# Kernel tuning notes

Hardware: AMD Instinct MI355X
Metric: run time of the kernel (lower is better)

## Reference

```python
import jax, jax.numpy as jnp
import numpy as np

NEG_SLOPE = 0.01  # torch nn.LeakyReLU default

B, N, IN_F, OUT_F, HEADS = 4, 2048, 512, 512, 8
D = OUT_F // HEADS  # 64


def setup_inputs() -> dict:
    key = jax.random.key(0)
    ks = jax.random.split(key, 4)
    X = jax.random.normal(ks[0], (B, N, IN_F), dtype=jnp.float32)
    W_v = jax.random.normal(ks[1], (IN_F, D), dtype=jnp.float32) * (IN_F ** -0.5)
    b_v = jnp.zeros((D,), dtype=jnp.float32)
    W_q = jax.random.normal(ks[2], (D, HEADS), dtype=jnp.float32) * (D ** -0.5)
    b_q = jnp.zeros((HEADS,), dtype=jnp.float32)
    W_k = jax.random.normal(ks[3], (D, HEADS), dtype=jnp.float32) * (D ** -0.5)
    b_k = jnp.zeros((HEADS,), dtype=jnp.float32)
    return {"X": X, "W_v": W_v, "b_v": b_v, "W_q": W_q, "b_q": b_q, "W_k": W_k, "b_k": b_k}


def reference(X, W_v, b_v, W_q, b_q, W_k, b_k):
    # V: (B, N, D)
    V = X @ W_v + b_v
    # per-node, per-head scalar scores: (B, N, H) -> (B, H, N)
    Q = jnp.swapaxes(V @ W_q + b_q, 1, 2)
    K = jnp.swapaxes(V @ W_k + b_k, 1, 2)
    # A[b,h,i,j] = leaky_relu(Q[b,h,j] + K[b,h,i])  (broadcast outer-sum)
    A = jax.nn.leaky_relu(Q[:, :, None, :] + K[:, :, :, None], negative_slope=NEG_SLOPE)
    A = jax.nn.softmax(A, axis=-1)  # dropout = identity in eval mode
    # H[b,i,h,f] = sum_j A[b,h,i,j] V[b,j,f]
    H = jnp.einsum('bhij,bjf->bihf', A, V)
    return H.reshape(H.shape[0], H.shape[1], -1)  # (B, N, H*D)
```

## Files before the change

### kernel.cpp

```cpp
#include <hip/hip_runtime.h>

#define BB   4
#define NN   2048
#define INF  512
#define HH   8
#define DD   64
#define BH   (BB*HH)
#define NCK  16
#define CKS  128
#define KSP  2


__global__ __launch_bounds__(256) void k_v(
    const float* __restrict__ X, const float* __restrict__ Wv,
    float* __restrict__ Vpart)
{
  __shared__ float Ws[64][68];
  const int t  = threadIdx.x;
  const int tc = t & 15;
  const int tr = t >> 4;
  const int rg = blockIdx.x >> 1;
  const int kh = blockIdx.x & 1;
  const int r0 = rg * 32;
  const int k0 = kh * 256;
  float acc[2][4] = {{0.f}};

  for (int kc = 0; kc < 256; kc += 64) {
    __syncthreads();
    #pragma unroll
    for (int i = 0; i < 4; i++) {
      const int e4 = t + i * 256;
      const int k  = e4 >> 4;
      const int n4 = (e4 & 15) * 4;
      *(float4*)(&Ws[k][n4]) = *(const float4*)(Wv + (size_t)(k0 + kc + k) * DD + n4);
    }
    __syncthreads();
    const float* xp0 = X + (size_t)(r0 + tr * 2) * INF + k0 + kc;
    const float* xp1 = xp0 + INF;
    #pragma unroll 8
    for (int kk = 0; kk < 64; kk += 4) {
      const float4 xa = *(const float4*)(xp0 + kk);
      const float4 xb = *(const float4*)(xp1 + kk);
      #pragma unroll
      for (int j = 0; j < 4; j++) {
        const float4 w4 = *(const float4*)(&Ws[kk + j][tc * 4]);
        const float xaj = (j == 0) ? xa.x : (j == 1) ? xa.y : (j == 2) ? xa.z : xa.w;
        const float xbj = (j == 0) ? xb.x : (j == 1) ? xb.y : (j == 2) ? xb.z : xb.w;
        acc[0][0] += xaj * w4.x;  acc[0][1] += xaj * w4.y;
        acc[0][2] += xaj * w4.z;  acc[0][3] += xaj * w4.w;
        acc[1][0] += xbj * w4.x;  acc[1][1] += xbj * w4.y;
        acc[1][2] += xbj * w4.z;  acc[1][3] += xbj * w4.w;
      }
    }
  }
  float* vp = Vpart + ((size_t)kh * (BB*NN) + r0 + tr * 2) * DD + tc * 4;
  #pragma unroll
  for (int r = 0; r < 2; r++) {
    float4 o;  o.x = acc[r][0];  o.y = acc[r][1];  o.z = acc[r][2];  o.w = acc[r][3];
    *(float4*)(vp + (size_t)r * DD) = o;
  }
}

__global__ __launch_bounds__(256) void k_vred(
    const float* __restrict__ Vpart, const float* __restrict__ bv,
    const float* __restrict__ Wq, const float* __restrict__ bq,
    const float* __restrict__ Wk, const float* __restrict__ bk,
    float* __restrict__ V, float* __restrict__ qsg, float* __restrict__ ksg)
{
  __shared__ float Vs[16][DD + 1];
  const int t  = threadIdx.x;
  const size_t e0 = ((size_t)blockIdx.x * 256 + t) * 4;
  const size_t STR = (size_t)BB * NN * DD;
  float4 a = *(const float4*)(Vpart + e0);
  #pragma unroll
  for (int p = 1; p < KSP; p++) {
    const float4 b = *(const float4*)(Vpart + (size_t)p * STR + e0);
    a.x += b.x;  a.y += b.y;  a.z += b.z;  a.w += b.w;
  }
  const float4 bb = *(const float4*)(bv + (e0 & 63));
  a.x += bb.x;  a.y += bb.y;  a.z += bb.z;  a.w += bb.w;
  *(float4*)(V + e0) = a;
  const int lrow = t >> 4;
  const int lcol = (t * 4) & 63;
  Vs[lrow][lcol]   = a.x;  Vs[lrow][lcol+1] = a.y;
  Vs[lrow][lcol+2] = a.z;  Vs[lrow][lcol+3] = a.w;
  __syncthreads();
  const int row = t >> 4;
  const int h   = t & 7;
  const bool isK = (t & 8) != 0;
  const float* W = isK ? Wk : Wq;
  float s = isK ? bk[h] : bq[h];
  #pragma unroll 8
  for (int dd = 0; dd < DD; dd++) s += Vs[row][dd] * W[dd*HH + h];
  const int grow = blockIdx.x * 16 + row;
  const int b = grow >> 11, n = grow & (NN - 1);
  (isK ? ksg : qsg)[(b*HH + h) * NN + n] = s;
}

__global__ __launch_bounds__(1024) void k_sort(
    float* __restrict__ q, unsigned short* __restrict__ idxg)
{
  __shared__ float key[NN];
  __shared__ int   idx[NN];
  const int t  = threadIdx.x;
  const int bh = blockIdx.x;
  key[t]        = q[bh*NN + t];        idx[t]        = t;
  key[t + 1024] = q[bh*NN + t + 1024]; idx[t + 1024] = t + 1024;
  __syncthreads();

#define CEX_STAGE(size, stride)                                         \
  {                                                                     \
    const int i = ((t & ~((stride) - 1)) << 1) | (t & ((stride) - 1));  \
    const int j = i + (stride);                                         \
    const bool up = ((i & (size)) == 0);                                \
    const float a = key[i], b = key[j];                                 \
    if (up ? (a > b) : (a < b)) {                                       \
      key[i] = b; key[j] = a;                                           \
      const int tmp = idx[i]; idx[i] = idx[j]; idx[j] = tmp;            \
    }                                                                   \
  }

  for (int size = 2; size <= 128; size <<= 1)
    for (int stride = size >> 1; stride > 0; stride >>= 1)
      CEX_STAGE(size, stride)
  __syncthreads();
  for (int size = 256; size <= 2048; size <<= 1) {
    for (int stride = size >> 1; stride >= 128; stride >>= 1) {
      CEX_STAGE(size, stride)
      __syncthreads();
    }
    for (int stride = 64; stride > 0; stride >>= 1)
      CEX_STAGE(size, stride)
    __syncthreads();
  }
#undef CEX_STAGE

  q[bh*NN + t]        = key[t];
  q[bh*NN + t + 1024] = key[t + 1024];
  idxg[bh*NN + t]        = (unsigned short)idx[t];
  idxg[bh*NN + t + 1024] = (unsigned short)idx[t + 1024];
}

__global__ __launch_bounds__(256) void k_scan(
    const float* __restrict__ sq, const unsigned short* __restrict__ idxg,
    const float* __restrict__ V,
    float* __restrict__ P1, float* __restrict__ P2,
    float* __restrict__ l1, float* __restrict__ l2,
    float* __restrict__ S1g, float* __restrict__ S2g,
    float* __restrict__ SL1, float* __restrict__ SL2)
{
  __shared__ float vstash[4][32][DD];
  __shared__ float ss1[4][64], ss2[4][64], sl1[4], sl2[4];
  const int t  = threadIdx.x;
  const int bh = blockIdx.x >> 4;
  const int ck = blockIdx.x & 15;
  const int d  = t & 63, g = t >> 6;
  const int r0 = ck*CKS + g*32;
  const float* Vb  = V + (size_t)(bh >> 3) * NN * DD;
  const float* sqb = sq + bh*NN;
  const unsigned short* ib = idxg + bh*NN;
  float a1 = 0.f, a2 = 0.f, s1 = 0.f, s2 = 0.f;
  #pragma unroll 8
  for (int rr = 0; rr < 32; rr++) {
    const int r = r0 + rr;
    const float qv = sqb[r];
    const float e1 = __expf(qv), e2 = __expf(0.01f*qv);
    const float v  = Vb[(size_t)ib[r]*DD + d];
    vstash[g][rr][d] = v;
    a1 += e1*v;  a2 += e2*v;  s1 += e1;  s2 += e2;
  }
  ss1[g][d] = a1;  ss2[g][d] = a2;
  if (d == 0) { sl1[g] = s1;  sl2[g] = s2; }
  __syncthreads();
  float o1 = 0.f, o2 = 0.f, lo1 = 0.f, lo2 = 0.f;
  for (int gg = 0; gg < g; gg++) { o1 += ss1[gg][d]; o2 += ss2[gg][d]; lo1 += sl1[gg]; lo2 += sl2[gg]; }
  if (g == 0) {
    S1g[(bh*NCK + ck)*64 + d] = ss1[0][d]+ss1[1][d]+ss1[2][d]+ss1[3][d];
    S2g[(bh*NCK + ck)*64 + d] = ss2[0][d]+ss2[1][d]+ss2[2][d]+ss2[3][d];
    if (d == 0) {
      SL1[bh*NCK + ck] = sl1[0]+sl1[1]+sl1[2]+sl1[3];
      SL2[bh*NCK + ck] = sl2[0]+sl2[1]+sl2[2]+sl2[3];
    }
  }
  a1 = o1; a2 = o2; s1 = lo1; s2 = lo2;
  float* P1b = P1 + (size_t)bh*NN*DD;
  float* P2b = P2 + (size_t)bh*NN*DD;
  #pragma unroll 8
  for (int rr = 0; rr < 32; rr++) {
    const int r = r0 + rr;
    const float qv = sqb[r];
    const float e1 = __expf(qv), e2 = __expf(0.01f*qv);
    const float v  = vstash[g][rr][d];
    P1b[(size_t)r*DD + d] = a1;
    P2b[(size_t)r*DD + d] = a2;
    if (d == 0) { l1[bh*NN + r] = s1;  l2[bh*NN + r] = s2; }
    a1 += e1*v;  a2 += e2*v;  s1 += e1;  s2 += e2;
  }
}

__global__ __launch_bounds__(256) void k_out(
    const float* __restrict__ sq, const float* __restrict__ ksg,
    const float* __restrict__ P1, const float* __restrict__ P2,
    const float* __restrict__ S1g, const float* __restrict__ S2g,
    const float* __restrict__ SL1, const float* __restrict__ SL2,
    const float* __restrict__ l1, const float* __restrict__ l2,
    float* __restrict__ out)
{
  __shared__ float Of1[NCK + 1][64], Of2[NCK + 1][64];
  __shared__ float Lo1[NCK + 1], Lo2[NCK + 1];
  const int t   = threadIdx.x;
  const int bh  = blockIdx.x >> 7;
  const int loc = blockIdx.x & 127;
  const int w   = t >> 6;
  const int d   = t & 63;
  const int i0  = loc*16 + w*4;
  const int b   = bh >> 3, h = bh & 7;

  if (t < 64) {
    float a = 0.f;
    for (int ck = 0; ck < NCK; ck++) {
      Of1[ck][t] = a;  a += S1g[(bh*NCK + ck)*64 + t];
    }
    Of1[NCK][t] = a;
  } else if (t < 128) {
    const int dd = t - 64;
    float a = 0.f;
    for (int ck = 0; ck < NCK; ck++) {
      Of2[ck][dd] = a;  a += S2g[(bh*NCK + ck)*64 + dd];
    }
    Of2[NCK][dd] = a;
  } else if (t == 128) {
    float a = 0.f;
    for (int ck = 0; ck < NCK; ck++) { Lo1[ck] = a;  a += SL1[bh*NCK + ck]; }
    Lo1[NCK] = a;
  } else if (t == 129) {
    float a = 0.f;
    for (int ck = 0; ck < NCK; ck++) { Lo2[ck] = a;  a += SL2[bh*NCK + ck]; }
    Lo2[NCK] = a;
  }
  __syncthreads();

  const float* s = sq + bh*NN;
  const float probe = s[d*32 + 31];
  const float T1  = Of1[NCK][d];
  const float Lt1 = Lo1[NCK];
  const size_t base = (size_t)bh * NN * DD;

  float kv[4], tt[4];
  int pos[4];
  #pragma unroll
  for (int u = 0; u < 4; u++) { kv[u] = ksg[bh*NN + i0 + u];  tt[u] = -kv[u]; }
  #pragma unroll
  for (int u = 0; u < 4; u++) {
    const unsigned long long m1 = __ballot(probe <= tt[u]);
    const int c1 = __popcll(m1);
    if (c1 == 64) pos[u] = NN;
    else {
      const unsigned long long m2 = __ballot(s[c1*32 + (d & 31)] <= tt[u]);
      pos[u] = c1*32 + (__popcll(m2) >> 1);
    }
  }
  #pragma unroll
  for (int u = 0; u < 4; u++) {
    const float ek  = __expf(kv[u]);
    const float ek2 = __expf(0.01f * kv[u]);
    float p1v, p2v, q1v, q2v;
    if (pos[u] < NN) {
      const int ch = pos[u] >> 7;
      p1v = P1[base + (size_t)pos[u]*DD + d] + Of1[ch][d];
      p2v = P2[base + (size_t)pos[u]*DD + d] + Of2[ch][d];
      q1v = l1[bh*NN + pos[u]] + Lo1[ch];
      q2v = l2[bh*NN + pos[u]] + Lo2[ch];
    } else {
      p1v = T1;   p2v = Of2[NCK][d];
      q1v = Lt1;  q2v = Lo2[NCK];
    }
    const float num = ek * (T1 - p1v)  + ek2 * p2v;
    const float den = ek * (Lt1 - q1v) + ek2 * q2v;
    out[((size_t)(b*NN + i0 + u)) * (HH*DD) + h*DD + d] = num / den;
  }
}

extern "C" void kernel_launch(void* const* d_in, const int* in_sizes, int n_in,
                              void* d_out, int out_size, void* d_ws, size_t ws_size,
                              hipStream_t stream)
{
  (void)in_sizes; (void)n_in; (void)out_size; (void)ws_size;
  const float* X  = (const float*)d_in[0];
  const float* Wv = (const float*)d_in[1];
  const float* bv = (const float*)d_in[2];
  const float* Wq = (const float*)d_in[3];
  const float* bq = (const float*)d_in[4];
  const float* Wk = (const float*)d_in[5];
  const float* bk = (const float*)d_in[6];
  float* out = (float*)d_out;

  float* w = (float*)d_ws;
  float* V     = w;  w += (size_t)BB*NN*DD;
  float* qsg   = w;  w += BH*NN;
  float* ksg   = w;  w += BH*NN;
  float* l1    = w;  w += BH*NN;
  float* l2    = w;  w += BH*NN;
  unsigned short* idxg = (unsigned short*)w;  w += BH*NN/2;
  float* S1g   = w;  w += (size_t)BH*NCK*DD;
  float* S2g   = w;  w += (size_t)BH*NCK*DD;
  float* SL1   = w;  w += BH*NCK;
  float* SL2   = w;  w += BH*NCK;
  float* P1    = w;  w += (size_t)BH*NN*DD;
  float* P2    = w;  w += (size_t)BH*NN*DD;

  float* Vpart = P1;

  k_v    <<<512, 256, 0, stream>>>(X, Wv, Vpart);
  k_vred <<<512, 256, 0, stream>>>(Vpart, bv, Wq, bq, Wk, bk, V, qsg, ksg);
  k_sort <<<BH, 1024, 0, stream>>>(qsg, idxg);
  k_scan <<<BH*NCK, 256, 0, stream>>>(qsg, idxg, V, P1, P2, l1, l2, S1g, S2g, SL1, SL2);
  k_out  <<<BH*128, 256, 0, stream>>>(qsg, ksg, P1, P2, S1g, S2g, SL1, SL2, l1, l2, out);
}
```

Baseline: 137.0 us.

## Replace per-head bitonic sort with rank-by-counting on packed 64-bit keys

The single-block-per-head bitonic sort (32 blocks of 1024 threads with many barriers) is replaced by a counting rank kernel. k_vred now emits order-preserving 64-bit keys that pack the transformed float bits with the node index, so every key is unique. Each thread then counts the keys smaller than its own over all 2048 and scatters its value and index to that rank. This trades O(N log^2 N) barrier-heavy shared-memory work on 32 blocks for O(N^2) cheap broadcast-load comparisons spread over 256 blocks, which raises parallelism but adds redundant global reads.

```diff
diff --git a/kernel.cpp b/kernel.cpp
--- a/kernel.cpp
+++ b/kernel.cpp
@@ -65,7 +65,8 @@
     const float* __restrict__ Vpart, const float* __restrict__ bv,
     const float* __restrict__ Wq, const float* __restrict__ bq,
     const float* __restrict__ Wk, const float* __restrict__ bk,
-    float* __restrict__ V, float* __restrict__ qsg, float* __restrict__ ksg)
+    float* __restrict__ V, float* __restrict__ qsg, float* __restrict__ ksg,
+    unsigned long long* __restrict__ qk64)
 {
   __shared__ float Vs[16][DD + 1];
   const int t  = threadIdx.x;
@@ -95,50 +96,42 @@
   const int grow = blockIdx.x * 16 + row;
   const int b = grow >> 11, n = grow & (NN - 1);
   (isK ? ksg : qsg)[(b*HH + h) * NN + n] = s;
-}
-
-__global__ __launch_bounds__(1024) void k_sort(
-    float* __restrict__ q, unsigned short* __restrict__ idxg)
-{
-  __shared__ float key[NN];
-  __shared__ int   idx[NN];
+  if (!isK) {
+    unsigned u = __float_as_uint(s);
+    u = (u & 0x80000000u) ? ~u : (u | 0x80000000u);
+    qk64[(size_t)(b*HH + h) * NN + n] =
+        ((unsigned long long)u << 32) | (unsigned)n;
+  }
+}
+
+__global__ __launch_bounds__(256) void k_rank(
+    const unsigned long long* __restrict__ qk64,
+    const float* __restrict__ q,
+    float* __restrict__ sqs, unsigned short* __restrict__ idxg)
+{
   const int t  = threadIdx.x;
-  const int bh = blockIdx.x;
-  key[t]        = q[bh*NN + t];        idx[t]        = t;
-  key[t + 1024] = q[bh*NN + t + 1024]; idx[t + 1024] = t + 1024;
-  __syncthreads();
-
-#define CEX_STAGE(size, stride)                                         \
-  {                                                                     \
-    const int i = ((t & ~((stride) - 1)) << 1) | (t & ((stride) - 1));  \
-    const int j = i + (stride);                                         \
-    const bool up = ((i & (size)) == 0);                                \
-    const float a = key[i], b = key[j];                                 \
-    if (up ? (a > b) : (a < b)) {                                       \
-      key[i] = b; key[j] = a;                                           \
-      const int tmp = idx[i]; idx[i] = idx[j]; idx[j] = tmp;            \
-    }                                                                   \
-  }
-
-  for (int size = 2; size <= 128; size <<= 1)
-    for (int stride = size >> 1; stride > 0; stride >>= 1)
-      CEX_STAGE(size, stride)
-  __syncthreads();
-  for (int size = 256; size <= 2048; size <<= 1) {
-    for (int stride = size >> 1; stride >= 128; stride >>= 1) {
-      CEX_STAGE(size, stride)
-      __syncthreads();
-    }
-    for (int stride = 64; stride > 0; stride >>= 1)
-      CEX_STAGE(size, stride)
-    __syncthreads();
-  }
-#undef CEX_STAGE
-
-  q[bh*NN + t]        = key[t];
-  q[bh*NN + t + 1024] = key[t + 1024];
-  idxg[bh*NN + t]        = (unsigned short)idx[t];
-  idxg[bh*NN + t + 1024] = (unsigned short)idx[t + 1024];
+  const int bh = blockIdx.x >> 3;
+  const int j  = ((blockIdx.x & 7) << 8) | t;
+  const unsigned long long* __restrict__ kb = qk64 + (size_t)bh * NN;
+  const unsigned long long kj = kb[j];
+  int c0 = 0, c1 = 0, c2 = 0, c3 = 0;
+  unsigned long long A[8], Bt[8];
+  #pragma unroll
+  for (int x = 0; x < 8; x++) A[x] = kb[x];
+  for (int l = 0; l < NN; l += 8) {
+    const int ln = (l + 8) & (NN - 1);
+    #pragma unroll
+    for (int x = 0; x < 8; x++) Bt[x] = kb[ln + x];
+    c0 += (A[0] < kj);  c1 += (A[1] < kj);
+    c2 += (A[2] < kj);  c3 += (A[3] < kj);
+    c0 += (A[4] < kj);  c1 += (A[5] < kj);
+    c2 += (A[6] < kj);  c3 += (A[7] < kj);
+    #pragma unroll
+    for (int x = 0; x < 8; x++) A[x] = Bt[x];
+  }
+  const int rank = (c0 + c1) + (c2 + c3);
+  sqs [bh*NN + rank] = q[bh*NN + j];
+  idxg[bh*NN + rank] = (unsigned short)j;
 }
 
 __global__ __launch_bounds__(256) void k_scan(
@@ -306,14 +299,16 @@
   float* S2g   = w;  w += (size_t)BH*NCK*DD;
   float* SL1   = w;  w += BH*NCK;
   float* SL2   = w;  w += BH*NCK;
+  float* sqs   = w;  w += BH*NN;
+  unsigned long long* qk64 = (unsigned long long*)w;  w += BH*NN*2;
   float* P1    = w;  w += (size_t)BH*NN*DD;
   float* P2    = w;  w += (size_t)BH*NN*DD;
 
   float* Vpart = P1;
 
   k_v    <<<512, 256, 0, stream>>>(X, Wv, Vpart);
-  k_vred <<<512, 256, 0, stream>>>(Vpart, bv, Wq, bq, Wk, bk, V, qsg, ksg);
-  k_sort <<<BH, 1024, 0, stream>>>(qsg, idxg);
-  k_scan <<<BH*NCK, 256, 0, stream>>>(qsg, idxg, V, P1, P2, l1, l2, S1g, S2g, SL1, SL2);
-  k_out  <<<BH*128, 256, 0, stream>>>(qsg, ksg, P1, P2, S1g, S2g, SL1, SL2, l1, l2, out);
-}
+  k_vred <<<512, 256, 0, stream>>>(Vpart, bv, Wq, bq, Wk, bk, V, qsg, ksg, qk64);
+  k_rank <<<BH*8, 256, 0, stream>>>(qk64, qsg, sqs, idxg);
+  k_scan <<<BH*NCK, 256, 0, stream>>>(sqs, idxg, V, P1, P2, l1, l2, S1g, S2g, SL1, SL2);
+  k_out  <<<BH*128, 256, 0, stream>>>(sqs, ksg, P1, P2, S1g, S2g, SL1, SL2, l1, l2, out);
+}
```

New measurement: 187.9 us. 1.37x slower.
